# Optimization experiments

Measured on AMD Instinct MI355X. Metric: run time of the kernel, lower is better.

## Reference

```python
import jax, jax.numpy as jnp
import numpy as np

# Convex_f forward. D and mid are fixed tridiagonal matrices:
#   (D x)[i]   = -x[i-1] + 2*x[i] - x[i+1]  for 1 <= i <= n-2, and 0 at i=0, n-1
#   (mid x)[i] = 0.5*(x[i-1] + x[i+1])      for 1 <= i <= n-2,
#                0.5*x[1] at i=0, 0.5*x[n-2] at i=n-1
# We implement these as direct 3-point stencils (same math as the dense matmuls).

B, N, K = 256, 8192, 16

def setup_inputs() -> dict:
    key = jax.random.key(0)
    k1, k2 = jax.random.split(key)
    x = jax.random.normal(k1, (B, N, K), dtype=jnp.float32)
    param = jax.random.normal(k2, (B, N, K), dtype=jnp.float32)
    return {"x": x, "param": param}

def _convex_step(y):
    # y: [B, N, K]
    up, ctr, dn = y[:, :-2], y[:, 1:-1], y[:, 2:]
    Dy_in = -up + 2.0 * ctr - dn                      # interior rows of D @ y
    Dy = jnp.pad(Dy_in, ((0, 0), (1, 1), (0, 0)))     # rows 0 and N-1 zeroed
    mid_y = jnp.concatenate(
        [0.5 * y[:, 1:2], 0.5 * (up + dn), 0.5 * y[:, -2:-1]], axis=1
    )                                                 # mid @ y
    dy = (Dy > 0).astype(y.dtype) * (y - mid_y)
    return y - dy

def reference(x, param):
    y = x + param
    return _convex_step(y) - param
```

## Files before the change

kernel.cpp:

```cpp
#include <hip/hip_runtime.h>


#define B_   256
#define N_   8192
#define KQ   4
#define R_   8
#define TPB  256
#define ROWS_PER_BLK ((TPB / KQ) * R_)
#define TILES (N_ / ROWS_PER_BLK)

static_assert(TILES == 16, "b = blk >> 4 assumes 16 tiles");

__device__ __forceinline__ float4 f4add(float4 a, float4 b) {
    return make_float4(a.x + b.x, a.y + b.y, a.z + b.z, a.w + b.w);
}

__global__ __launch_bounds__(TPB)
void convex_kernel(const float4* __restrict__ x4,
                   const float4* __restrict__ p4,
                   float4* __restrict__ o4)
{
    const int tid = threadIdx.x;
    const int c   = tid & (KQ - 1);
    const int g   = tid >> 2;
    const int blk = blockIdx.x;
    const int t   = blk & (TILES - 1);
    const int b   = blk >> 4;
    const int n0  = t * ROWS_PER_BLK + g * R_;

    const int base = (b * N_ + n0) * KQ + c;

    const int topI = (n0 > 0)        ? base - KQ       : base;
    const int botI = (n0 + R_ < N_)  ? base + R_ * KQ  : base;

    float4 xt = x4[topI];
    float4 pt = p4[topI];
    float4 xb = x4[botI];
    float4 pb = p4[botI];

    float4 xv[R_], pv[R_];
#pragma unroll
    for (int j = 0; j < R_; ++j) {
        xv[j] = x4[base + j * KQ];
        pv[j] = p4[base + j * KQ];
    }

    float4 y[R_ + 2];
    y[0] = f4add(xt, pt);
#pragma unroll
    for (int j = 0; j < R_; ++j) y[j + 1] = f4add(xv[j], pv[j]);
    y[R_ + 1] = f4add(xb, pb);

#pragma unroll
    for (int j = 0; j < R_; ++j) {
        const int n = n0 + j;
        const float4 yc = y[j + 1];
        const float4 p  = pv[j];
        float4 r;
        if (n == 0 || n == N_ - 1) {
            r = make_float4(yc.x - p.x, yc.y - p.y, yc.z - p.z, yc.w - p.w);
        } else {
            const float4 a = y[j];
            const float4 d = y[j + 2];
            const float4 m = make_float4(0.5f * (a.x + d.x), 0.5f * (a.y + d.y),
                                         0.5f * (a.z + d.z), 0.5f * (a.w + d.w));
            r = make_float4(fminf(yc.x, m.x) - p.x,
                            fminf(yc.y, m.y) - p.y,
                            fminf(yc.z, m.z) - p.z,
                            fminf(yc.w, m.w) - p.w);
        }
        o4[base + j * KQ] = r;
    }
}

extern "C" void kernel_launch(void* const* d_in, const int* in_sizes, int n_in,
                              void* d_out, int out_size, void* d_ws, size_t ws_size,
                              hipStream_t stream)
{
    const float4* x = (const float4*)d_in[0];
    const float4* p = (const float4*)d_in[1];
    float4*       o = (float4*)d_out;

    dim3 grid(B_ * TILES);
    dim3 block(TPB);
    convex_kernel<<<grid, block, 0, stream>>>(x, p, o);
}
```

Baseline: 308.9 us.

## Coalesce row loads per wave with LDS halo exchange and nontemporal stores

Each wave now owns a contiguous span of 64 rows. A lane loads rows strided by 16, so each load instruction reads one contiguous 1 KB chunk instead of scattered 128-byte pieces. Neighbour values for the stencil are exchanged through shared memory with a wave barrier, and only edge lanes fetch the halo rows, cutting redundant halo loads. Output goes through nontemporal stores to avoid polluting the cache, at the cost of LDS traffic and extra divergence on the halo lanes.

```diff
diff --git a/kernel.cpp b/kernel.cpp
--- a/kernel.cpp
+++ b/kernel.cpp
@@ -1,18 +1,28 @@
 #include <hip/hip_runtime.h>
 
 
-#define B_   256
-#define N_   8192
-#define KQ   4
-#define R_   8
-#define TPB  256
-#define ROWS_PER_BLK ((TPB / KQ) * R_)
+#define B_    256
+#define N_    8192
+#define KQ    4
+#define R_    4
+#define WROWS (16 * R_)
+#define TPB   256
+#define WAVES (TPB / 64)
+#define ROWS_PER_BLK (WROWS * WAVES)
 #define TILES (N_ / ROWS_PER_BLK)
 
-static_assert(TILES == 16, "b = blk >> 4 assumes 16 tiles");
+static_assert(TILES == 32, "b = blk >> 5 assumes 32 tiles");
+
+typedef float nfloat4 __attribute__((ext_vector_type(4)));
 
 __device__ __forceinline__ float4 f4add(float4 a, float4 b) {
     return make_float4(a.x + b.x, a.y + b.y, a.z + b.z, a.w + b.w);
+}
+
+__device__ __forceinline__ void nt_store(float4* p, float4 v) {
+    nfloat4 nv;
+    nv.x = v.x; nv.y = v.y; nv.z = v.z; nv.w = v.w;
+    __builtin_nontemporal_store(nv, reinterpret_cast<nfloat4*>(p));
 }
 
 __global__ __launch_bounds__(TPB)
@@ -20,48 +30,60 @@
                    const float4* __restrict__ p4,
                    float4* __restrict__ o4)
 {
+    __shared__ float4 lds[WAVES][WROWS + 2][KQ];
+
     const int tid = threadIdx.x;
-    const int c   = tid & (KQ - 1);
-    const int g   = tid >> 2;
+    const int w   = tid >> 6;
+    const int l   = tid & 63;
+    const int g   = l >> 2;
+    const int c   = l & 3;
     const int blk = blockIdx.x;
     const int t   = blk & (TILES - 1);
-    const int b   = blk >> 4;
-    const int n0  = t * ROWS_PER_BLK + g * R_;
+    const int b   = blk >> 5;
+    const int wrow0 = t * ROWS_PER_BLK + w * WROWS;
 
-    const int base = (b * N_ + n0) * KQ + c;
+    const int base = (b * N_ + wrow0 + g) * KQ + c;
 
-    const int topI = (n0 > 0)        ? base - KQ       : base;
-    const int botI = (n0 + R_ < N_)  ? base + R_ * KQ  : base;
-
-    float4 xt = x4[topI];
-    float4 pt = p4[topI];
-    float4 xb = x4[botI];
-    float4 pb = p4[botI];
+    const bool topL = (l < 4);
+    const bool botL = (l >= 60);
+    float4 hxv, hpv;
+    if (topL | botL) {
+        int hidx = topL ? (base - ((wrow0 > 0) ? KQ : 0))
+                        : (base + ((wrow0 + WROWS < N_) ? (WROWS - 15) * KQ : 0));
+        hxv = x4[hidx];
+        hpv = p4[hidx];
+    }
 
     float4 xv[R_], pv[R_];
 #pragma unroll
     for (int j = 0; j < R_; ++j) {
-        xv[j] = x4[base + j * KQ];
-        pv[j] = p4[base + j * KQ];
+        xv[j] = x4[base + j * 16 * KQ];
+        pv[j] = p4[base + j * 16 * KQ];
     }
 
-    float4 y[R_ + 2];
-    y[0] = f4add(xt, pt);
+    float4 y[R_];
 #pragma unroll
-    for (int j = 0; j < R_; ++j) y[j + 1] = f4add(xv[j], pv[j]);
-    y[R_ + 1] = f4add(xb, pb);
+    for (int j = 0; j < R_; ++j) {
+        y[j] = f4add(xv[j], pv[j]);
+        lds[w][1 + g + j * 16][c] = y[j];
+    }
+    if (topL | botL) {
+        lds[w][topL ? 0 : (WROWS + 1)][c] = f4add(hxv, hpv);
+    }
+
+    __builtin_amdgcn_wave_barrier();
 
 #pragma unroll
     for (int j = 0; j < R_; ++j) {
-        const int n = n0 + j;
-        const float4 yc = y[j + 1];
+        const int n = wrow0 + j * 16 + g;
+        const float4 yc = y[j];
         const float4 p  = pv[j];
         float4 r;
         if (n == 0 || n == N_ - 1) {
             r = make_float4(yc.x - p.x, yc.y - p.y, yc.z - p.z, yc.w - p.w);
         } else {
-            const float4 a = y[j];
-            const float4 d = y[j + 2];
+            const float4 a = lds[w][g + j * 16][c];
+            const float4 d = lds[w][2 + g + j * 16][c];
             const float4 m = make_float4(0.5f * (a.x + d.x), 0.5f * (a.y + d.y),
                                          0.5f * (a.z + d.z), 0.5f * (a.w + d.w));
             r = make_float4(fminf(yc.x, m.x) - p.x,
@@ -69,7 +91,7 @@
                             fminf(yc.z, m.z) - p.z,
                             fminf(yc.w, m.w) - p.w);
         }
-        o4[base + j * KQ] = r;
+        nt_store(&o4[base + j * 16 * KQ], r);
     }
 }
 
```

Result: no change. 314.6 us (+1.9%).

## Stream rows per wave with coalesced loads and shuffle-based stencil neighbours

Applied to the files above, without the earlier changes.

Replaces the per-thread 8-row tiles, whose loads were strided across the wave, with a persistent wave-per-span loop in which each iteration reads a contiguous 1 KB slab. Neighbouring rows are exchanged with wave shuffles and carried between iterations, which removes the redundant halo reloads. Loads are prefetched two iterations ahead. The grid shrinks to 1024 blocks, which may limit memory-level parallelism.

```diff
diff --git a/kernel.cpp b/kernel.cpp
--- a/kernel.cpp
+++ b/kernel.cpp
@@ -4,15 +4,22 @@
 #define B_   256
 #define N_   8192
 #define KQ   4
-#define R_   8
 #define TPB  256
-#define ROWS_PER_BLK ((TPB / KQ) * R_)
-#define TILES (N_ / ROWS_PER_BLK)
+#define GRID 1024
+#define NWAVES (GRID * (TPB / 64))
+#define SPAN 512
+#define NT   (SPAN / 16)
+#define TS   (16 * KQ)
 
-static_assert(TILES == 16, "b = blk >> 4 assumes 16 tiles");
+static_assert((long)B_ * N_ == (long)NWAVES * SPAN, "span math");
+static_assert(N_ % SPAN == 0, "spans must not cross batch boundary");
 
 __device__ __forceinline__ float4 f4add(float4 a, float4 b) {
     return make_float4(a.x + b.x, a.y + b.y, a.z + b.z, a.w + b.w);
+}
+__device__ __forceinline__ float4 shfl4(float4 v, int src) {
+    return make_float4(__shfl(v.x, src, 64), __shfl(v.y, src, 64),
+                       __shfl(v.z, src, 64), __shfl(v.w, src, 64));
 }
 
 __global__ __launch_bounds__(TPB)
@@ -21,55 +28,77 @@
                    float4* __restrict__ o4)
 {
     const int tid = threadIdx.x;
-    const int c   = tid & (KQ - 1);
-    const int g   = tid >> 2;
-    const int blk = blockIdx.x;
-    const int t   = blk & (TILES - 1);
-    const int b   = blk >> 4;
-    const int n0  = t * ROWS_PER_BLK + g * R_;
+    const int w   = tid >> 6;
+    const int l   = tid & 63;
+    const int g   = l >> 2;
+    const int c   = l & 3;
+    const int wid = blockIdx.x * (TPB / 64) + w;
+    const int b   = wid >> 4;
+    const int ns  = (wid & 15) * SPAN;
 
-    const int base = (b * N_ + n0) * KQ + c;
+    const int base0 = (b * N_ + ns + g) * KQ + c;
 
-    const int topI = (n0 > 0)        ? base - KQ       : base;
-    const int botI = (n0 + R_ < N_)  ? base + R_ * KQ  : base;
-
-    float4 xt = x4[topI];
-    float4 pt = p4[topI];
-    float4 xb = x4[botI];
-    float4 pb = p4[botI];
-
-    float4 xv[R_], pv[R_];
-#pragma unroll
-    for (int j = 0; j < R_; ++j) {
-        xv[j] = x4[base + j * KQ];
-        pv[j] = p4[base + j * KQ];
+    float4 t        = make_float4(0.f, 0.f, 0.f, 0.f);
+    float4 last_bot = make_float4(0.f, 0.f, 0.f, 0.f);
+    if (l < 4) {
+        const int hr = (ns > 0) ? ns - 1 : ns;
+        const int hi = (b * N_ + hr) * KQ + c;
+        t = f4add(x4[hi], p4[hi]);
+    }
+    if (l >= 60) {
+        const int br = (ns + SPAN < N_) ? ns + SPAN : N_ - 1;
+        const int bi = (b * N_ + br) * KQ + c;
+        last_bot = f4add(x4[bi], p4[bi]);
     }
 
-    float4 y[R_ + 2];
-    y[0] = f4add(xt, pt);
-#pragma unroll
-    for (int j = 0; j < R_; ++j) y[j + 1] = f4add(xv[j], pv[j]);
-    y[R_ + 1] = f4add(xb, pb);
+    float4 xa = x4[base0];
+    float4 pa = p4[base0];
+    float4 xn = x4[base0 + TS];
+    float4 pn = p4[base0 + TS];
+    float4 y    = f4add(xa, pa);
+    float4 pcur = pa;
 
-#pragma unroll
-    for (int j = 0; j < R_; ++j) {
-        const int n = n0 + j;
-        const float4 yc = y[j + 1];
-        const float4 p  = pv[j];
+    const int upL = l - 4;
+    const int dnL = l + 4;
+    const int tL  = 60 + c;
+    const int bL  = c;
+
+#pragma unroll 4
+    for (int i = 0; i < NT; ++i) {
+        const int qi = (i + 2 < NT) ? i + 2 : NT - 1;
+        float4 xq = x4[base0 + qi * TS];
+        float4 pq = p4[base0 + qi * TS];
+
+        float4 yn = f4add(xn, pn);
+
+        float4 bot = shfl4(yn, bL);
+        if (i == NT - 1) bot = last_bot;
+
+        float4 a = shfl4(y, upL);
+        float4 d = shfl4(y, dnL);
+        if (g == 0)  a = t;
+        if (g == 15) d = bot;
+
+        const int n = ns + i * 16 + g;
         float4 r;
         if (n == 0 || n == N_ - 1) {
-            r = make_float4(yc.x - p.x, yc.y - p.y, yc.z - p.z, yc.w - p.w);
+            r = make_float4(y.x - pcur.x, y.y - pcur.y,
+                            y.z - pcur.z, y.w - pcur.w);
         } else {
-            const float4 a = y[j];
-            const float4 d = y[j + 2];
             const float4 m = make_float4(0.5f * (a.x + d.x), 0.5f * (a.y + d.y),
                                          0.5f * (a.z + d.z), 0.5f * (a.w + d.w));
-            r = make_float4(fminf(yc.x, m.x) - p.x,
-                            fminf(yc.y, m.y) - p.y,
-                            fminf(yc.z, m.z) - p.z,
-                            fminf(yc.w, m.w) - p.w);
+            r = make_float4(fminf(y.x, m.x) - pcur.x,
+                            fminf(y.y, m.y) - pcur.y,
+                            fminf(y.z, m.z) - pcur.z,
+                            fminf(y.w, m.w) - pcur.w);
         }
-        o4[base + j * KQ] = r;
+        o4[base0 + i * TS] = r;
+
+        t    = shfl4(y, tL);
+        y    = yn;
+        pcur = pn;
+        xn   = xq;
+        pn   = pq;
     }
 }
 
@@ -81,7 +110,7 @@
     const float4* p = (const float4*)d_in[1];
     float4*       o = (float4*)d_out;
 
-    dim3 grid(B_ * TILES);
+    dim3 grid(GRID);
     dim3 block(TPB);
     convex_kernel<<<grid, block, 0, stream>>>(x, p, o);
 }
```

Result: no change. 312.3 us (+1.1%).
